# Optimization experiments

Measured on AMD Instinct MI355X. Metric: run time of the kernel, lower is better.

The kernel has to match this reference:

```python
import jax, jax.numpy as jnp
import numpy as np

N_NODES = 100000
N_EDGES = 640000
D_FEAT = 128


def setup_inputs() -> dict:
    key = jax.random.key(0)
    k1, k2, k3, k4 = jax.random.split(key, 4)
    input = jax.random.normal(k1, (N_NODES, D_FEAT), dtype=jnp.float32)
    eidx = jax.random.randint(k2, (2, N_EDGES), 0, N_NODES, dtype=jnp.int64)
    enorm = jax.random.uniform(k3, (N_EDGES,), dtype=jnp.float32)
    esgn = jnp.sign(jax.random.normal(k4, (N_EDGES,), dtype=jnp.float32))
    return {"input": input, "eidx": eidx, "enorm": enorm, "esgn": esgn}


def reference(input, eidx, enorm, esgn):
    # gather source features, scale by sign*norm, scatter-add into targets
    sidx, tidx = eidx[0], eidx[1]
    message = input[sidx] * (esgn * enorm)[:, None]  # [E, D]
    res = jax.ops.segment_sum(message, tidx, num_segments=input.shape[0])
    return res
```

## Files before the change

kernel.cpp:

```cpp
#include <hip/hip_runtime.h>
#include <hip/hip_bf16.h>

#define D_FEAT  128
#define CAP     16
#define OVFCAP  65536
#define CHUNK   512


__device__ __forceinline__ unsigned short f32_to_bf16_rne(float x) {
    union { float f; unsigned int u; } v; v.f = x;
    unsigned int r = v.u + 0x7fffu + ((v.u >> 16) & 1u);
    return (unsigned short)(r >> 16);
}

__device__ __forceinline__ unsigned pack_rec(int s, float w) {
    unsigned sign = (__float_as_uint(w) >> 31) & 1u;
    float a = fabsf(w);
    int q = __float2int_rn(a * 16383.0f);
    if (q > 16383) q = 16383;
    return ((unsigned)s << 15) | (sign << 14) | (unsigned)q;
}

__global__ __launch_bounds__(256) void convfill_kernel(
    const float* __restrict__ in,
    const int* __restrict__ sidx, const int* __restrict__ tidx,
    const float* __restrict__ enorm, const float* __restrict__ esgn,
    unsigned short* __restrict__ bhalf,
    int* __restrict__ cnt,
    unsigned* __restrict__ bucket,
    int4* __restrict__ ovf,
    int R, int edgeBlocks, int cstride, int nConvThreads, int nE, int nN)
{
    int bid = (int)blockIdx.x;
    int er  = bid / R;
    bool isEdge = ((bid % R) == 0) && (er < edgeBlocks);

    if (isEdge) {
        int base = er * 512 + (int)threadIdx.x;
        int t0 = -1, t1 = -1, s0 = 0, s1 = 0;
        float w0 = 0.f, w1 = 0.f;
        int e0 = base, e1 = base + 256;
        if (e0 < nE) { t0 = tidx[e0]; s0 = sidx[e0]; w0 = esgn[e0] * enorm[e0]; }
        if (e1 < nE) { t1 = tidx[e1]; s1 = sidx[e1]; w1 = esgn[e1] * enorm[e1]; }
        int p0 = 0, p1 = 0;
        if (t0 >= 0) p0 = atomicAdd(&cnt[(size_t)t0 * cstride], 1);
        if (t1 >= 0) p1 = atomicAdd(&cnt[(size_t)t1 * cstride], 1);
        if (t0 >= 0) {
            if (p0 < CAP) bucket[(size_t)t0 * CAP + p0] = pack_rec(s0, w0);
            else {
                int q = atomicAdd(&cnt[(size_t)nN * cstride], 1);
                if (q < OVFCAP) ovf[q] = make_int4(s0, t0, __float_as_int(w0), 0);
            }
        }
        if (t1 >= 0) {
            if (p1 < CAP) bucket[(size_t)t1 * CAP + p1] = pack_rec(s1, w1);
            else {
                int q = atomicAdd(&cnt[(size_t)nN * cstride], 1);
                if (q < OVFCAP) ovf[q] = make_int4(s1, t1, __float_as_int(w1), 0);
            }
        }
    } else {
        int convIdx = bid - min(er + 1, edgeBlocks);
        int i = convIdx * 256 + (int)threadIdx.x;
        if (i >= nConvThreads) return;
        const float4* ip = reinterpret_cast<const float4*>(in) + (size_t)i * 2;
        float4 a = ip[0];
        float4 b = ip[1];
        union { int4 q; unsigned short u[8]; } o;
        o.u[0] = f32_to_bf16_rne(a.x); o.u[1] = f32_to_bf16_rne(a.y);
        o.u[2] = f32_to_bf16_rne(a.z); o.u[3] = f32_to_bf16_rne(a.w);
        o.u[4] = f32_to_bf16_rne(b.x); o.u[5] = f32_to_bf16_rne(b.y);
        o.u[6] = f32_to_bf16_rne(b.z); o.u[7] = f32_to_bf16_rne(b.w);
        reinterpret_cast<int4*>(bhalf)[i] = o.q;
    }
}

__global__ __launch_bounds__(256) void gather_bf16(
    const unsigned short* __restrict__ bhalf,
    const int*  __restrict__ cnt,
    const unsigned* __restrict__ bucket,
    const int4* __restrict__ ovf,
    float* __restrict__ out, int cstride, int nN)
{
    long long gid = (long long)blockIdx.x * blockDim.x + threadIdx.x;
    int node = (int)(gid >> 4);
    int lane = (int)(gid & 15);
    if (node >= nN) return;

    int degRaw = cnt[(size_t)node * cstride];
    int deg = degRaw > CAP ? CAP : degRaw;

    unsigned myrec = bucket[(size_t)node * CAP + lane];
    int wl = threadIdx.x & 63;
    int gbase = wl & 48;

    float a0 = 0.f, a1 = 0.f, a2 = 0.f, a3 = 0.f;
    float a4 = 0.f, a5 = 0.f, a6 = 0.f, a7 = 0.f;

    #define ROW_ACC(Sv, Wv)                                                     \
    do {                                                                        \
        const int4* rp = reinterpret_cast<const int4*>(                         \
            bhalf + (size_t)(Sv) * D_FEAT);                                     \
        int4 q = rp[lane];                                                      \
        float w_ = (Wv);                                                        \
        unsigned int x0 = (unsigned int)q.x, x1 = (unsigned int)q.y;            \
        unsigned int x2 = (unsigned int)q.z, x3 = (unsigned int)q.w;            \
        a0 += __int_as_float((int)(x0 << 16)) * w_;                             \
        a1 += __int_as_float((int)(x0 & 0xffff0000u)) * w_;                     \
        a2 += __int_as_float((int)(x1 << 16)) * w_;                             \
        a3 += __int_as_float((int)(x1 & 0xffff0000u)) * w_;                     \
        a4 += __int_as_float((int)(x2 << 16)) * w_;                             \
        a5 += __int_as_float((int)(x2 & 0xffff0000u)) * w_;                     \
        a6 += __int_as_float((int)(x3 << 16)) * w_;                             \
        a7 += __int_as_float((int)(x3 & 0xffff0000u)) * w_;                     \
    } while (0)

    #define DECODE(r, Sv, Wv)                                                   \
        int Sv = (int)((r) >> 15);                                              \
        float Wv = (float)((r) & 0x3fffu) * (1.0f / 16383.0f);                  \
        Wv = ((r) & 0x4000u) ? -Wv : Wv;

    int j = 0;
    for (; j + 4 <= deg; j += 4) {
        unsigned r0 = (unsigned)__shfl((int)myrec, gbase + j + 0, 64);
        unsigned r1 = (unsigned)__shfl((int)myrec, gbase + j + 1, 64);
        unsigned r2 = (unsigned)__shfl((int)myrec, gbase + j + 2, 64);
        unsigned r3 = (unsigned)__shfl((int)myrec, gbase + j + 3, 64);
        DECODE(r0, s0, w0); DECODE(r1, s1, w1);
        DECODE(r2, s2, w2); DECODE(r3, s3, w3);
        ROW_ACC(s0, w0);
        ROW_ACC(s1, w1);
        ROW_ACC(s2, w2);
        ROW_ACC(s3, w3);
    }
    for (; j < deg; ++j) {
        unsigned r0 = (unsigned)__shfl((int)myrec, gbase + j, 64);
        DECODE(r0, s0, w0);
        ROW_ACC(s0, w0);
    }

    if (degRaw > CAP) {
        int novf = cnt[(size_t)nN * cstride];
        if (novf > OVFCAP) novf = OVFCAP;
        for (int k = 0; k < novf; ++k) {
            int4 r = ovf[k];
            if (r.y == node) ROW_ACC(r.x, __int_as_float(r.z));
        }
    }
    #undef DECODE
    #undef ROW_ACC

    float* orow = out + (size_t)node * D_FEAT + (size_t)lane * 8;
    reinterpret_cast<float4*>(orow)[0] = make_float4(a0, a1, a2, a3);
    reinterpret_cast<float4*>(orow)[1] = make_float4(a4, a5, a6, a7);
}


__global__ __launch_bounds__(256) void fill_bucket(
    const int* __restrict__ sidx, const int* __restrict__ tidx,
    const float* __restrict__ enorm, const float* __restrict__ esgn,
    int* __restrict__ cnt, int2* __restrict__ bucket,
    int4* __restrict__ ovf, int nE, int nN)
{
    int e = blockIdx.x * blockDim.x + threadIdx.x;
    if (e >= nE) return;
    int t = tidx[e];
    int s = sidx[e];
    float w = esgn[e] * enorm[e];
    int pos = atomicAdd(&cnt[t], 1);
    if (pos < CAP) {
        bucket[(size_t)t * CAP + pos] = make_int2(s, __float_as_int(w));
    } else {
        int p = atomicAdd(&cnt[nN], 1);
        ovf[p] = make_int4(s, t, __float_as_int(w), 0);
    }
}

__global__ __launch_bounds__(256) void gather_bucket(
    const float* __restrict__ in, const int* __restrict__ cnt,
    const int2* __restrict__ bucket, float* __restrict__ out, int nNodes)
{
    long long gid = (long long)blockIdx.x * blockDim.x + threadIdx.x;
    int node = (int)(gid >> 4);
    int lane = (int)(gid & 15);
    if (node >= nNodes) return;

    int deg = cnt[node];
    if (deg > CAP) deg = CAP;
    const int2* eb = bucket + (size_t)node * CAP;

    float4 a0 = make_float4(0.f, 0.f, 0.f, 0.f);
    float4 a1 = make_float4(0.f, 0.f, 0.f, 0.f);
    int j = 0;
    for (; j + 2 <= deg; j += 2) {
        int2 e0 = eb[j];
        int2 e1 = eb[j + 1];
        const float4* r0 = reinterpret_cast<const float4*>(in + (size_t)e0.x * D_FEAT);
        const float4* r1 = reinterpret_cast<const float4*>(in + (size_t)e1.x * D_FEAT);
        float4 v00 = r0[lane];
        float4 v01 = r0[lane + 16];
        float4 v10 = r1[lane];
        float4 v11 = r1[lane + 16];
        float w0 = __int_as_float(e0.y);
        float w1 = __int_as_float(e1.y);
        a0.x += v00.x * w0; a0.y += v00.y * w0; a0.z += v00.z * w0; a0.w += v00.w * w0;
        a1.x += v01.x * w0; a1.y += v01.y * w0; a1.z += v01.z * w0; a1.w += v01.w * w0;
        a0.x += v10.x * w1; a0.y += v10.y * w1; a0.z += v10.z * w1; a0.w += v10.w * w1;
        a1.x += v11.x * w1; a1.y += v11.y * w1; a1.z += v11.z * w1; a1.w += v11.w * w1;
    }
    if (j < deg) {
        int2 e0 = eb[j];
        const float4* r0 = reinterpret_cast<const float4*>(in + (size_t)e0.x * D_FEAT);
        float4 v00 = r0[lane];
        float4 v01 = r0[lane + 16];
        float w0 = __int_as_float(e0.y);
        a0.x += v00.x * w0; a0.y += v00.y * w0; a0.z += v00.z * w0; a0.w += v00.w * w0;
        a1.x += v01.x * w0; a1.y += v01.y * w0; a1.z += v01.z * w0; a1.w += v01.w * w0;
    }
    float4* orow = reinterpret_cast<float4*>(out + (size_t)node * D_FEAT);
    orow[lane]      = a0;
    orow[lane + 16] = a1;
}

__global__ __launch_bounds__(256) void ovf_scatter(
    const float* __restrict__ in, const int* __restrict__ cnt,
    const int4* __restrict__ ovf, float* __restrict__ out, int nN)
{
    int novf = cnt[nN];
    long long total = (long long)novf * 32;
    long long stride = (long long)gridDim.x * blockDim.x;
    for (long long gid = (long long)blockIdx.x * blockDim.x + threadIdx.x;
         gid < total; gid += stride) {
        int e = (int)(gid >> 5);
        int lane = (int)(gid & 31);
        int4 r = ovf[e];
        float w = __int_as_float(r.z);
        float4 v = reinterpret_cast<const float4*>(in + (size_t)r.x * D_FEAT)[lane];
        float* dst = out + (size_t)r.y * D_FEAT + (size_t)lane * 4;
        atomicAdd(dst + 0, v.x * w);
        atomicAdd(dst + 1, v.y * w);
        atomicAdd(dst + 2, v.z * w);
        atomicAdd(dst + 3, v.w * w);
    }
}


__global__ __launch_bounds__(256) void hist_kernel(
    const int* __restrict__ tidx, int* __restrict__ cnt, int nE)
{
    int e = blockIdx.x * blockDim.x + threadIdx.x;
    if (e < nE) atomicAdd(&cnt[tidx[e]], 1);
}

__global__ __launch_bounds__(CHUNK) void scan_chunks(
    const int* __restrict__ cnt, int* __restrict__ offs,
    int* __restrict__ bsums, int n)
{
    __shared__ int sh[CHUNK];
    int i = blockIdx.x * CHUNK + threadIdx.x;
    int v = (i < n) ? cnt[i] : 0;
    sh[threadIdx.x] = v;
    __syncthreads();
    for (int d = 1; d < CHUNK; d <<= 1) {
        int t = sh[threadIdx.x];
        int u = (threadIdx.x >= d) ? sh[threadIdx.x - d] : 0;
        __syncthreads();
        sh[threadIdx.x] = t + u;
        __syncthreads();
    }
    int incl = sh[threadIdx.x];
    if (i < n) offs[i] = incl - v;
    if (threadIdx.x == CHUNK - 1) bsums[blockIdx.x] = incl;
}

__global__ __launch_bounds__(256) void scan_bsums(
    int* __restrict__ bsums, int nb)
{
    __shared__ int sh[256];
    int v = (threadIdx.x < nb) ? bsums[threadIdx.x] : 0;
    sh[threadIdx.x] = v;
    __syncthreads();
    for (int d = 1; d < 256; d <<= 1) {
        int t = sh[threadIdx.x];
        int u = (threadIdx.x >= d) ? sh[threadIdx.x - d] : 0;
        __syncthreads();
        sh[threadIdx.x] = t + u;
        __syncthreads();
    }
    if (threadIdx.x < nb) bsums[threadIdx.x] = sh[threadIdx.x] - v;
}

__global__ __launch_bounds__(256) void fill_csr(
    const int* __restrict__ sidx, const int* __restrict__ tidx,
    const float* __restrict__ enorm, const float* __restrict__ esgn,
    int* __restrict__ offs, const int* __restrict__ bsums,
    int2* __restrict__ edges, int nE)
{
    int e = blockIdx.x * blockDim.x + threadIdx.x;
    if (e >= nE) return;
    int t = tidx[e];
    int pos = bsums[t >> 9] + atomicAdd(&offs[t], 1);
    float w = esgn[e] * enorm[e];
    edges[pos] = make_int2(sidx[e], __float_as_int(w));
}

__global__ __launch_bounds__(256) void gather_kernel(
    const float* __restrict__ in, const int* __restrict__ offs,
    const int* __restrict__ bsums, const int2* __restrict__ edges,
    float* __restrict__ out, int nNodes)
{
    long long gid = (long long)blockIdx.x * blockDim.x + threadIdx.x;
    int node = (int)(gid >> 4);
    int lane = (int)(gid & 15);
    if (node >= nNodes) return;

    int base = bsums[node >> 9];
    int beg  = base + ((node & 511) ? offs[node - 1] : 0);
    int end  = base + offs[node];

    float4 a0 = make_float4(0.f, 0.f, 0.f, 0.f);
    float4 a1 = make_float4(0.f, 0.f, 0.f, 0.f);
    for (int j = beg; j < end; ++j) {
        int2 e0 = edges[j];
        const float4* r0 = reinterpret_cast<const float4*>(in + (size_t)e0.x * D_FEAT);
        float4 v00 = r0[lane];
        float4 v01 = r0[lane + 16];
        float w0 = __int_as_float(e0.y);
        a0.x += v00.x * w0; a0.y += v00.y * w0; a0.z += v00.z * w0; a0.w += v00.w * w0;
        a1.x += v01.x * w0; a1.y += v01.y * w0; a1.z += v01.z * w0; a1.w += v01.w * w0;
    }
    float4* orow = reinterpret_cast<float4*>(out + (size_t)node * D_FEAT);
    orow[lane]      = a0;
    orow[lane + 16] = a1;
}

__global__ __launch_bounds__(256) void graphconv_scatter(
    const float* __restrict__ in, const int* __restrict__ sidx,
    const int* __restrict__ tidx, const float* __restrict__ enorm,
    const float* __restrict__ esgn, float* __restrict__ out, int nE)
{
    long long gid = (long long)blockIdx.x * blockDim.x + threadIdx.x;
    int edge = (int)(gid >> 5);
    int lane = (int)(gid & 31);
    if (edge >= nE) return;
    int s = sidx[edge];
    int t = tidx[edge];
    float w = esgn[edge] * enorm[edge];
    float4 v = reinterpret_cast<const float4*>(in + (size_t)s * D_FEAT)[lane];
    float* dst = out + (size_t)t * D_FEAT + (size_t)lane * 4;
    atomicAdd(dst + 0, v.x * w);
    atomicAdd(dst + 1, v.y * w);
    atomicAdd(dst + 2, v.z * w);
    atomicAdd(dst + 3, v.w * w);
}

extern "C" void kernel_launch(void* const* d_in, const int* in_sizes, int n_in,
                              void* d_out, int out_size, void* d_ws, size_t ws_size,
                              hipStream_t stream) {
    const float* input = (const float*)d_in[0];
    const int*   eidx  = (const int*)d_in[1];
    const float* enorm = (const float*)d_in[2];
    const float* esgn  = (const float*)d_in[3];
    float* out = (float*)d_out;

    const int nE = in_sizes[2];
    const int nN = out_size / D_FEAT;
    const int* sidx = eidx;
    const int* tidx = eidx + nE;

    int eg = (nE + 255) / 256;

    size_t bhalf_bytes = (size_t)nN * D_FEAT * 2;
    size_t bucketA_b   = (size_t)nN * CAP * 4;
    size_t ovfA_b      = (size_t)OVFCAP * 16;
    int cstride = 0;
    size_t cnt_bytes = 0;
    if (nN <= (1 << 17)) {
        for (int cs : {16, 4, 1}) {
            size_t cb = ((size_t)nN * cs + 1) * 4;
            size_t na = bhalf_bytes + bucketA_b + ovfA_b + cb;
            if (ws_size >= na) { cstride = cs; cnt_bytes = cb; break; }
        }
    }

    size_t bucketB_b = (size_t)nN * CAP * 8;
    size_t ovfB_b    = (size_t)nE * 16;
    size_t cntB_b    = ((size_t)nN + 1) * 4;
    size_t need_B    = bucketB_b + ovfB_b + cntB_b;

    const int nb = (nN + CHUNK - 1) / CHUNK;
    size_t need_C = ((size_t)nN + 256 + 2 * (size_t)nE) * 4;

    if (cstride > 0) {
        unsigned short* bhalf = (unsigned short*)d_ws;
        unsigned* bucket = (unsigned*)((char*)d_ws + bhalf_bytes);
        int4*     ovf    = (int4*)((char*)d_ws + bhalf_bytes + bucketA_b);
        int*      cnt    = (int*)((char*)d_ws + bhalf_bytes + bucketA_b + ovfA_b);

        hipMemsetAsync(cnt, 0, cnt_bytes, stream);

        int nConvThreads = nN * (D_FEAT / 8);
        int convBlocks = (nConvThreads + 255) / 256;
        int edgeBlocks = (nE + 511) / 512;
        int totBlocks  = convBlocks + edgeBlocks;
        int R = totBlocks / edgeBlocks;
        if (R < 1) R = 1;
        convfill_kernel<<<totBlocks, 256, 0, stream>>>(
            input, sidx, tidx, enorm, esgn, bhalf, cnt, bucket, ovf,
            R, edgeBlocks, cstride, nConvThreads, nE, nN);

        long long gthreads = (long long)nN * 16;
        int ggrid = (int)((gthreads + 255) / 256);
        gather_bf16<<<ggrid, 256, 0, stream>>>(bhalf, cnt, bucket, ovf, out,
                                               cstride, nN);
    } else if (ws_size >= need_B) {
        int2* bucket = (int2*)d_ws;
        int4* ovf    = (int4*)((char*)d_ws + bucketB_b);
        int*  cnt    = (int*)((char*)d_ws + bucketB_b + ovfB_b);

        hipMemsetAsync(cnt, 0, cntB_b, stream);
        fill_bucket<<<eg, 256, 0, stream>>>(sidx, tidx, enorm, esgn,
                                            cnt, bucket, ovf, nE, nN);
        long long gthreads = (long long)nN * 16;
        int ggrid = (int)((gthreads + 255) / 256);
        gather_bucket<<<ggrid, 256, 0, stream>>>(input, cnt, bucket, out, nN);
        ovf_scatter<<<256, 256, 0, stream>>>(input, cnt, ovf, out, nN);
    } else if (ws_size >= need_C && nb <= 256) {
        int*  offs  = (int*)d_ws;
        int*  bsums = offs + nN;
        int2* edges = (int2*)(bsums + 256);

        hipMemsetAsync(offs, 0, (size_t)nN * 4, stream);
        hist_kernel<<<eg, 256, 0, stream>>>(tidx, offs, nE);
        scan_chunks<<<nb, CHUNK, 0, stream>>>(offs, offs, bsums, nN);
        scan_bsums<<<1, 256, 0, stream>>>(bsums, nb);
        fill_csr<<<eg, 256, 0, stream>>>(sidx, tidx, enorm, esgn,
                                         offs, bsums, edges, nE);
        long long gthreads = (long long)nN * 16;
        int ggrid = (int)((gthreads + 255) / 256);
        gather_kernel<<<ggrid, 256, 0, stream>>>(input, offs, bsums, edges,
                                                 out, nN);
    } else {
        hipMemsetAsync(d_out, 0, (size_t)out_size * 4, stream);
        long long tthreads = (long long)nE * 32;
        int grid = (int)((tthreads + 255) / 256);
        graphconv_scatter<<<grid, 256, 0, stream>>>(input, sidx, tidx, enorm,
                                                    esgn, out, nE);
    }
}
```

Baseline: 86.02 us.

## Fuse edge bucketing and bf16 conversion per thread instead of interleaved block roles

The fused convert/fill kernel stops giving each block a single role (an edge block every R blocks, conversion blocks otherwise). Every thread now handles one edge: it issues the count atomic, then does its bf16 conversion of 8 features, then writes the bucket record, so the conversion work hides the atomic latency. With 1.6M conversion threads and 640K edges, only the first blocks carry edge work, so the load is uneven across blocks.

```diff
diff --git a/kernel.cpp b/kernel.cpp
--- a/kernel.cpp
+++ b/kernel.cpp
@@ -29,41 +29,22 @@
     int* __restrict__ cnt,
     unsigned* __restrict__ bucket,
     int4* __restrict__ ovf,
-    int R, int edgeBlocks, int cstride, int nConvThreads, int nE, int nN)
-{
-    int bid = (int)blockIdx.x;
-    int er  = bid / R;
-    bool isEdge = ((bid % R) == 0) && (er < edgeBlocks);
-
-    if (isEdge) {
-        int base = er * 512 + (int)threadIdx.x;
-        int t0 = -1, t1 = -1, s0 = 0, s1 = 0;
-        float w0 = 0.f, w1 = 0.f;
-        int e0 = base, e1 = base + 256;
-        if (e0 < nE) { t0 = tidx[e0]; s0 = sidx[e0]; w0 = esgn[e0] * enorm[e0]; }
-        if (e1 < nE) { t1 = tidx[e1]; s1 = sidx[e1]; w1 = esgn[e1] * enorm[e1]; }
-        int p0 = 0, p1 = 0;
-        if (t0 >= 0) p0 = atomicAdd(&cnt[(size_t)t0 * cstride], 1);
-        if (t1 >= 0) p1 = atomicAdd(&cnt[(size_t)t1 * cstride], 1);
-        if (t0 >= 0) {
-            if (p0 < CAP) bucket[(size_t)t0 * CAP + p0] = pack_rec(s0, w0);
-            else {
-                int q = atomicAdd(&cnt[(size_t)nN * cstride], 1);
-                if (q < OVFCAP) ovf[q] = make_int4(s0, t0, __float_as_int(w0), 0);
-            }
-        }
-        if (t1 >= 0) {
-            if (p1 < CAP) bucket[(size_t)t1 * CAP + p1] = pack_rec(s1, w1);
-            else {
-                int q = atomicAdd(&cnt[(size_t)nN * cstride], 1);
-                if (q < OVFCAP) ovf[q] = make_int4(s1, t1, __float_as_int(w1), 0);
-            }
-        }
-    } else {
-        int convIdx = bid - min(er + 1, edgeBlocks);
-        int i = convIdx * 256 + (int)threadIdx.x;
-        if (i >= nConvThreads) return;
-        const float4* ip = reinterpret_cast<const float4*>(in) + (size_t)i * 2;
+    int cstride, int nConvThreads, int nE, int nN)
+{
+    int gid = (int)blockIdx.x * 256 + (int)threadIdx.x;
+
+    int t = -1, s = 0;
+    float w = 0.f;
+    int p = 0;
+    if (gid < nE) {
+        t = tidx[gid];
+        s = sidx[gid];
+        w = esgn[gid] * enorm[gid];
+        p = atomicAdd(&cnt[(size_t)t * cstride], 1);
+    }
+
+    if (gid < nConvThreads) {
+        const float4* ip = reinterpret_cast<const float4*>(in) + (size_t)gid * 2;
         float4 a = ip[0];
         float4 b = ip[1];
         union { int4 q; unsigned short u[8]; } o;
@@ -71,7 +52,16 @@
         o.u[2] = f32_to_bf16_rne(a.z); o.u[3] = f32_to_bf16_rne(a.w);
         o.u[4] = f32_to_bf16_rne(b.x); o.u[5] = f32_to_bf16_rne(b.y);
         o.u[6] = f32_to_bf16_rne(b.z); o.u[7] = f32_to_bf16_rne(b.w);
-        reinterpret_cast<int4*>(bhalf)[i] = o.q;
+        reinterpret_cast<int4*>(bhalf)[gid] = o.q;
+    }
+
+    if (t >= 0) {
+        if (p < CAP) {
+            bucket[(size_t)t * CAP + p] = pack_rec(s, w);
+        } else {
+            int q = atomicAdd(&cnt[(size_t)nN * cstride], 1);
+            if (q < OVFCAP) ovf[q] = make_int4(s, t, __float_as_int(w), 0);
+        }
     }
 }
 
@@ -401,13 +391,10 @@
 
         int nConvThreads = nN * (D_FEAT / 8);
         int convBlocks = (nConvThreads + 255) / 256;
-        int edgeBlocks = (nE + 511) / 512;
-        int totBlocks  = convBlocks + edgeBlocks;
-        int R = totBlocks / edgeBlocks;
-        if (R < 1) R = 1;
+        int totBlocks  = max(convBlocks, eg);
         convfill_kernel<<<totBlocks, 256, 0, stream>>>(
             input, sidx, tidx, enorm, esgn, bhalf, cnt, bucket, ovf,
-            R, edgeBlocks, cstride, nConvThreads, nE, nN);
+            cstride, nConvThreads, nE, nN);
 
         long long gthreads = (long long)nN * 16;
         int ggrid = (int)((gthreads + 255) / 256);
```

Measured after the change: 88.16 us. 1.02x slower.
